# Kernel optimization log

Hardware: AMD Instinct MI355X
Metric: run time of the kernel (lower is better)

## Reference

```python
import jax, jax.numpy as jnp
import numpy as np

B, S, D = 64, 512, 768
NEG = -1e30


def setup_inputs() -> dict:
    key = jax.random.key(0)
    ks = jax.random.split(key, 20)
    def rn(k, shape, scale=0.02):
        return jax.random.normal(k, shape, dtype=jnp.float32) * scale
    ep = jax.random.randint(ks[1], (B, 3, 2), 0, S, dtype=jnp.int32)
    return {
        "encoding": jax.random.normal(ks[0], (B, S, D), dtype=jnp.float32),
        "ent_pos": jnp.sort(ep, axis=-1),
        "Ar_W": rn(ks[2], (5, D)), "Ar_b": rn(ks[3], (D,)),
        "Vr_W1": rn(ks[4], (2 * D, 512)), "Vr_b1": rn(ks[5], (512,)),
        "Vr_W2": rn(ks[6], (512, 5)), "Vr_b2": rn(ks[7], (5,)),
        "gate_W": rn(ks[8], (2 * D, D)), "gate_b": rn(ks[9], (D,)),
        "pred_W1": rn(ks[10], (3 * D, 512)), "pred_b1": rn(ks[11], (512,)),
        "pred_W2": rn(ks[12], (512, 5)), "pred_b2": rn(ks[13], (5,)),
        "proj_W": rn(ks[14], (D, 1)), "proj_b": rn(ks[15], (1,)),
    }


def reference(encoding, ent_pos, Ar_W, Ar_b, Vr_W1, Vr_b1, Vr_W2, Vr_b2,
              gate_W, gate_b, pred_W1, pred_b1, pred_W2, pred_b2, proj_W, proj_b):
    # --- entity span max-pooling (vectorized over batch & 3 entities) ---
    pos = jnp.arange(S)                                   # [S]
    start = ent_pos[..., 0:1]                             # [B,3,1]
    end = ent_pos[..., 1:2]                               # [B,3,1]
    mask = (pos >= start) & (pos <= end)                  # [B,3,S]
    ent = jnp.max(jnp.where(mask[..., None], encoding[:, None, :, :], NEG), axis=2)  # [B,3,D]
    # dropout layers are identity at inference

    def vr(a, b):  # V_r_layer: Linear(1536,512)+ReLU+Linear(512,5)+Sigmoid
        h = jax.nn.relu(jnp.concatenate([a, b], axis=-1) @ Vr_W1 + Vr_b1)
        return jax.nn.sigmoid(h @ Vr_W2 + Vr_b2)          # [B,5]

    def gate(u, e):  # gated residual update
        g = jax.nn.sigmoid(jnp.concatenate([u, e], axis=-1) @ gate_W + gate_b)
        return g * e + (1.0 - g) * u

    e1, e2, e3 = ent[:, 0], ent[:, 1], ent[:, 2]          # [B,D] each
    for _ in range(5):
        u1 = (vr(e2, e3) @ Ar_W + Ar_b) * e1
        u2 = (vr(e1, e3) @ Ar_W + Ar_b) * e2
        u3 = (vr(e1, e2) @ Ar_W + Ar_b) * e3
        e1, e2, e3 = gate(u1, e1), gate(u2, e2), gate(u3, e3)
    final_ent = jnp.stack([e1, e2, e3], axis=1)           # [B,3,D]

    # predict_layer on the ORIGINAL pooled entity embeddings (per source code)
    flat = ent.reshape(B, 3 * D)
    rel = jax.nn.relu(flat @ pred_W1 + pred_b1) @ pred_W2 + pred_b2  # [B,5]
    ent_score = jax.nn.sigmoid(ent @ proj_W + proj_b)[..., 0]       # [B,3]
    return rel, ent_score, final_ent
```

## Files before the change

kernel.cpp:

```cpp
#include <hip/hip_runtime.h>
#include <hip/hip_bf16.h>
#include <math.h>

#define NEGF (-1e30f)

#define P_OFF   0u
#define ENT_OFF 1179648u
#define EA_OFF  1327104u
#define EB_OFF  1474560u
#define SP_OFF  1622016u
#define PP_OFF  1637376u

__device__ __forceinline__ float sigmoidf_(float x){ return 1.0f/(1.0f+expf(-x)); }

__global__ __launch_bounds__(192) void k_spanmax_partial(
    const float* __restrict__ enc, const int* __restrict__ ent_pos, float* __restrict__ ws)
{
    int bi = blockIdx.y; int c = blockIdx.x; int t = threadIdx.x;
    int b = bi/3;
    int st = ent_pos[bi*2+0], en = ent_pos[bi*2+1];
    int r0 = max(st, c*64), r1 = min(en, c*64+63);
    float4 m = make_float4(NEGF,NEGF,NEGF,NEGF);
    const float4* e4 = (const float4*)enc + (size_t)b*512*192 + t;
    int r = r0;
    for (; r+3<=r1; r+=4){
        float4 v0 = e4[(size_t)(r  )*192];
        float4 v1 = e4[(size_t)(r+1)*192];
        float4 v2 = e4[(size_t)(r+2)*192];
        float4 v3 = e4[(size_t)(r+3)*192];
        m.x=fmaxf(m.x,fmaxf(fmaxf(v0.x,v1.x),fmaxf(v2.x,v3.x)));
        m.y=fmaxf(m.y,fmaxf(fmaxf(v0.y,v1.y),fmaxf(v2.y,v3.y)));
        m.z=fmaxf(m.z,fmaxf(fmaxf(v0.z,v1.z),fmaxf(v2.z,v3.z)));
        m.w=fmaxf(m.w,fmaxf(fmaxf(v0.w,v1.w),fmaxf(v2.w,v3.w)));
    }
    for (; r<=r1; ++r){
        float4 v = e4[(size_t)r*192];
        m.x=fmaxf(m.x,v.x); m.y=fmaxf(m.y,v.y); m.z=fmaxf(m.z,v.z); m.w=fmaxf(m.w,v.w);
    }
    ((float4*)(ws+P_OFF))[(bi*8+c)*192 + t] = m;
}

__global__ __launch_bounds__(256) void k_spanmax_reduce(
    const float* __restrict__ projW, const float* __restrict__ projb,
    float* __restrict__ ws, float* __restrict__ out)
{
    __shared__ float red[256];
    int bi = blockIdx.x; int t = threadIdx.x;
    float local = 0.f;
    if (t < 192){
        float4 m = make_float4(NEGF,NEGF,NEGF,NEGF);
        const float4* p4 = (const float4*)(ws+P_OFF);
        for (int c=0;c<8;++c){
            float4 v = p4[(bi*8+c)*192+t];
            m.x=fmaxf(m.x,v.x); m.y=fmaxf(m.y,v.y); m.z=fmaxf(m.z,v.z); m.w=fmaxf(m.w,v.w);
        }
        ((float4*)(ws+ENT_OFF))[bi*192+t] = m;
        ((float4*)(ws+EA_OFF))[bi*192+t] = m;
        float4 w = ((const float4*)projW)[t];
        local = m.x*w.x + m.y*w.y + m.z*w.z + m.w*w.w;
    }
    red[t]=local; __syncthreads();
    for (int off=128; off>0; off>>=1){ if (t<off) red[t]+=red[t+off]; __syncthreads(); }
    if (t==0) out[320 + bi] = sigmoidf_(red[0] + projb[0]);
}

__global__ __launch_bounds__(256) void k_pred_part(
    const float* __restrict__ predW1, float* __restrict__ ws)
{
    int ct = blockIdx.x, rb = blockIdx.y, ks = blockIdx.z;
    int tx = threadIdx.x & 31, ty = threadIdx.x >> 5;
    int row = rb*8+ty, col = ct*32+tx;
    const float* A = ws + ENT_OFF + (size_t)row*2304 + ks*288;
    const float* W = predW1 + (size_t)(ks*288)*512 + col;
    float acc = 0.f;
    #pragma unroll 4
    for (int k=0;k<288;++k){ acc = fmaf(A[k], W[(size_t)k*512], acc); }
    ws[PP_OFF + ((size_t)(ks*64+row))*512 + col] = acc;
}

__global__ __launch_bounds__(256) void k_pred_fin(
    const float* __restrict__ pb1, const float* __restrict__ predW2,
    const float* __restrict__ pb2, float* __restrict__ ws, float* __restrict__ out)
{
    __shared__ float ph[512];
    __shared__ float red[256];
    int b = blockIdx.x, t = threadIdx.x;
    for (int c = t; c < 512; c += 256){
        float s = 0.f;
        for (int ks=0;ks<8;++ks) s += ws[PP_OFF + ((size_t)(ks*64+b))*512 + c];
        ph[c] = fmaxf(s + pb1[c], 0.f);
    }
    __syncthreads();
    for (int c=0;c<5;++c){
        float local = ph[t]*predW2[t*5+c] + ph[t+256]*predW2[(t+256)*5+c];
        red[t]=local; __syncthreads();
        for (int off=128; off>0; off>>=1){ if (t<off) red[t]+=red[t+off]; __syncthreads(); }
        if (t==0) out[b*5+c] = red[0] + pb2[c];
        __syncthreads();
    }
}

__global__ __launch_bounds__(256) void k_vr_fused(
    const float* __restrict__ W1, const float* __restrict__ b1,
    const float* __restrict__ W2, const float* __restrict__ eSrc,
    float* __restrict__ ws)
{
    __shared__ float eL[4608];
    __shared__ float red[16*16*17];
    int ct = blockIdx.x, bg = blockIdx.y;
    int t = threadIdx.x;
    int b0 = bg*2;
    const float* eBase = eSrc + (size_t)b0*2304;
    for (int idx=t; idx<4608; idx+=256) eL[idx] = eBase[idx];
    __syncthreads();

    int tp = t & 15;
    int kq = t >> 4;
    int c0 = ct*64;
    int col = c0 + 4*tp;
    const float* Wp = W1 + (size_t)(kq*96)*512 + col;
    int off1 = (kq<8) ? (768 + kq*96) : (1536 + (kq-8)*96);
    int off2 = (kq<8) ? (      kq*96) : (768  + (kq-8)*96);
    const float* pP0 = eL + off1;
    const float* pQ0 = eL + off2;
    const float* pP1 = eL + 2304 + off1;
    const float* pQ1 = eL + 2304 + off2;
    float aP0[4]={0,0,0,0}, aQ0[4]={0,0,0,0}, aP1[4]={0,0,0,0}, aQ1[4]={0,0,0,0};
    #pragma unroll 8
    for (int i=0;i<96;++i){
        float4 w = *(const float4*)(Wp + (size_t)i*512);
        float p0 = pP0[i], q0 = pQ0[i], p1 = pP1[i], q1 = pQ1[i];
        aP0[0]=fmaf(p0,w.x,aP0[0]); aP0[1]=fmaf(p0,w.y,aP0[1]); aP0[2]=fmaf(p0,w.z,aP0[2]); aP0[3]=fmaf(p0,w.w,aP0[3]);
        aQ0[0]=fmaf(q0,w.x,aQ0[0]); aQ0[1]=fmaf(q0,w.y,aQ0[1]); aQ0[2]=fmaf(q0,w.z,aQ0[2]); aQ0[3]=fmaf(q0,w.w,aQ0[3]);
        aP1[0]=fmaf(p1,w.x,aP1[0]); aP1[1]=fmaf(p1,w.y,aP1[1]); aP1[2]=fmaf(p1,w.z,aP1[2]); aP1[3]=fmaf(p1,w.w,aP1[3]);
        aQ1[0]=fmaf(q1,w.x,aQ1[0]); aQ1[1]=fmaf(q1,w.y,aQ1[1]); aQ1[2]=fmaf(q1,w.z,aQ1[2]); aQ1[3]=fmaf(q1,w.w,aQ1[3]);
    }
    float* rp = red + (kq*16 + tp)*17;
    #pragma unroll
    for (int c=0;c<4;++c){ rp[c]=aP0[c]; rp[4+c]=aQ0[c]; rp[8+c]=aP1[c]; rp[12+c]=aQ1[c]; }
    __syncthreads();

    if (t < 128){
        int bb = t >> 6;
        int tc = t & 63;
        int tp2 = tc >> 2, c = tc & 3;
        int base = bb*8;
        float SP1=0,SP2=0,SQ1=0,SQ2=0;
        #pragma unroll
        for (int k=0;k<8;++k){
            SP1 += red[(k*16+tp2)*17 + base + c];
            SQ1 += red[(k*16+tp2)*17 + base + 4 + c];
            SP2 += red[((k+8)*16+tp2)*17 + base + c];
            SQ2 += red[((k+8)*16+tp2)*17 + base + 4 + c];
        }
        int cc = c0 + tc;
        float bv = b1[cc];
        float h0 = fmaxf(SP1+SP2+bv, 0.f);
        float h1 = fmaxf(SQ1+SP2+bv, 0.f);
        float h2 = fmaxf(SQ1+SQ2+bv, 0.f);
        float w20 = W2[cc*5+0], w21 = W2[cc*5+1], w22 = W2[cc*5+2], w23 = W2[cc*5+3], w24 = W2[cc*5+4];
        float pr[15] = { h0*w20,h0*w21,h0*w22,h0*w23,h0*w24,
                         h1*w20,h1*w21,h1*w22,h1*w23,h1*w24,
                         h2*w20,h2*w21,h2*w22,h2*w23,h2*w24 };
        #pragma unroll
        for (int j=0;j<15;++j){
            float v = pr[j];
            v += __shfl_down(v, 32);
            v += __shfl_down(v, 16);
            v += __shfl_down(v, 8);
            v += __shfl_down(v, 4);
            v += __shfl_down(v, 2);
            v += __shfl_down(v, 1);
            pr[j] = v;
        }
        if (tc == 0){
            float* sp = ws + SP_OFF + ((size_t)ct*192 + (size_t)(b0+bb)*3)*5;
            #pragma unroll
            for (int j=0;j<15;++j) sp[j] = pr[j];
        }
    }
}

__global__ __launch_bounds__(256) void k_gate_fused(
    const float* __restrict__ gW, const float* __restrict__ gb,
    const float* __restrict__ ArW, const float* __restrict__ Arb,
    const float* __restrict__ Vb2,
    const float* __restrict__ eSrc, float* __restrict__ eDst,
    float* __restrict__ ws, float* __restrict__ finalOut)
{
    __shared__ float eL[4608];
    __shared__ float uL[4608];
    __shared__ float red[16*16*25];
    __shared__ float sL[32];
    int ct = blockIdx.x, bg = blockIdx.y;
    int t = threadIdx.x;
    int b0 = bg*2;
    const float* eBase = eSrc + (size_t)b0*2304;
    for (int idx=t; idx<4608; idx+=256) eL[idx] = eBase[idx];
    if (t < 30){
        int bb = t/15, pc = t%15, cc = pc%5;
        int row = (b0+bb)*3 + pc/5;
        float pre = Vb2[cc];
        #pragma unroll
        for (int q=0;q<8;++q) pre += ws[SP_OFF + ((size_t)q*192 + row)*5 + cc];
        sL[t] = sigmoidf_(pre);
    }
    __syncthreads();
    for (int idx=t; idx<4608; idx+=256){
        int r = idx / 768;
        int k = idx - r*768;
        int bb = r / 3;  int p = r - bb*3;
        const float* s = sL + bb*15 + p*5;
        float a = Arb[k] + s[0]*ArW[k] + s[1]*ArW[768+k] + s[2]*ArW[1536+k]
                         + s[3]*ArW[2304+k] + s[4]*ArW[3072+k];
        uL[idx] = a * eL[idx];
    }
    __syncthreads();

    int tp = t & 15, kq = t >> 4;
    int c0 = ct*64;
    int col = c0 + 4*tp;
    const float* Wp = gW + (size_t)(kq*96)*768 + col;
    const float* A = (kq<8) ? uL : eL;
    int kb = (kq & 7)*96;
    float acc[6][4];
    #pragma unroll
    for (int r=0;r<6;++r){ acc[r][0]=0.f; acc[r][1]=0.f; acc[r][2]=0.f; acc[r][3]=0.f; }
    #pragma unroll 4
    for (int i=0;i<96;++i){
        float4 w = *(const float4*)(Wp + (size_t)i*768);
        #pragma unroll
        for (int r=0;r<6;++r){
            float a = A[r*768 + kb + i];
            acc[r][0] = fmaf(a, w.x, acc[r][0]);
            acc[r][1] = fmaf(a, w.y, acc[r][1]);
            acc[r][2] = fmaf(a, w.z, acc[r][2]);
            acc[r][3] = fmaf(a, w.w, acc[r][3]);
        }
    }
    float* rp = red + (kq*16+tp)*25;
    #pragma unroll
    for (int r=0;r<6;++r){
        rp[r*4+0]=acc[r][0]; rp[r*4+1]=acc[r][1]; rp[r*4+2]=acc[r][2]; rp[r*4+3]=acc[r][3];
    }
    __syncthreads();

    for (int o=t; o<384; o+=256){
        int tc = o & 63, rr = o >> 6;
        int tp2 = tc >> 2, c = tc & 3;
        int bb = rr/3, p = rr - bb*3;
        float gp = 0.f;
        #pragma unroll
        for (int k=0;k<16;++k) gp += red[(k*16+tp2)*25 + rr*4 + c];
        int jc = c0 + tc;
        float g = sigmoidf_(gp + gb[jc]);
        float e = eL[bb*2304 + p*768 + jc];
        float u = uL[bb*2304 + p*768 + jc];
        float val = g*e + (1.f-g)*u;
        size_t oi = ((size_t)(b0+bb)*3 + p)*768 + jc;
        eDst[oi] = val;
        if (finalOut) finalOut[oi] = val;
    }
}

extern "C" void kernel_launch(void* const* d_in, const int* in_sizes, int n_in,
                              void* d_out, int out_size, void* d_ws, size_t ws_size,
                              hipStream_t stream)
{
    const float* enc     = (const float*)d_in[0];
    const int*   ent_pos = (const int*)d_in[1];
    const float* ArW     = (const float*)d_in[2];
    const float* Arb     = (const float*)d_in[3];
    const float* VrW1    = (const float*)d_in[4];
    const float* Vrb1    = (const float*)d_in[5];
    const float* VrW2    = (const float*)d_in[6];
    const float* Vrb2    = (const float*)d_in[7];
    const float* gateW   = (const float*)d_in[8];
    const float* gateb   = (const float*)d_in[9];
    const float* predW1  = (const float*)d_in[10];
    const float* predb1  = (const float*)d_in[11];
    const float* predW2  = (const float*)d_in[12];
    const float* predb2  = (const float*)d_in[13];
    const float* projW   = (const float*)d_in[14];
    const float* projb   = (const float*)d_in[15];
    float* out = (float*)d_out;
    float* ws  = (float*)d_ws;

    hipLaunchKernelGGL(k_spanmax_partial, dim3(8,192), dim3(192), 0, stream, enc, ent_pos, ws);
    hipLaunchKernelGGL(k_spanmax_reduce, dim3(192), dim3(256), 0, stream, projW, projb, ws, out);
    hipLaunchKernelGGL(k_pred_part, dim3(16,8,8), dim3(256), 0, stream, predW1, ws);
    hipLaunchKernelGGL(k_pred_fin, dim3(64), dim3(256), 0, stream, predb1, predW2, predb2, ws, out);
    for (int it=0; it<5; ++it){
        float* eS = ws + ((it&1)==0 ? EA_OFF : EB_OFF);
        float* eD = ws + ((it&1)==0 ? EB_OFF : EA_OFF);
        hipLaunchKernelGGL(k_vr_fused,   dim3(8,32),  dim3(256), 0, stream, VrW1, Vrb1, VrW2, eS, ws);
        hipLaunchKernelGGL(k_gate_fused, dim3(12,32), dim3(256), 0, stream, gateW, gateb, ArW, Arb, Vrb2,
                           eS, eD, ws, (it==4) ? (out+512) : (float*)nullptr);
    }
}
```

Before: 165.0 us.

## Fuse all stages into one persistent cooperative kernel with grid syncs

Replaces the 14 separate kernel launches (span max, reduce, pred part/fin, and five vr/gate iterations) with a single cooperative kernel of 256 blocks of 512 threads that uses grid.sync between phases. The pred MLP is restructured so each block handles 4 batches by a 128-column strip and completes the second layer locally, and the gate phase now covers 128 columns per block with 192 blocks. The aim is to remove launch gaps between many small dependent kernels. The cost is fewer blocks (one per CU), grid-wide barriers, and idle blocks in phases that use only 64 or 192 of them.

After: 575.9 us. 249% more time.

```diff
diff --git a/kernel.cpp b/kernel.cpp
--- a/kernel.cpp
+++ b/kernel.cpp
@@ -1,265 +1,301 @@
 #include <hip/hip_runtime.h>
-#include <hip/hip_bf16.h>
+#include <hip/hip_cooperative_groups.h>
 #include <math.h>
 
+namespace cg = cooperative_groups;
+
 #define NEGF (-1e30f)
 
-#define P_OFF   0u
-#define ENT_OFF 1179648u
-#define EA_OFF  1327104u
-#define EB_OFF  1474560u
-#define SP_OFF  1622016u
-#define PP_OFF  1637376u
+#define P_OFF    0u
+#define ENT_OFF  1179648u
+#define EA_OFF   1327104u
+#define EB_OFF   1474560u
+#define SP_OFF   1622016u
+#define PRED_OFF 1629696u
 
 __device__ __forceinline__ float sigmoidf_(float x){ return 1.0f/(1.0f+expf(-x)); }
 
-__global__ __launch_bounds__(192) void k_spanmax_partial(
-    const float* __restrict__ enc, const int* __restrict__ ent_pos, float* __restrict__ ws)
+__global__ __launch_bounds__(512, 1) void k_mega(
+    const float* __restrict__ enc, const int* __restrict__ ent_pos,
+    const float* __restrict__ ArW, const float* __restrict__ Arb,
+    const float* __restrict__ VrW1, const float* __restrict__ Vrb1,
+    const float* __restrict__ VrW2, const float* __restrict__ Vrb2,
+    const float* __restrict__ gW, const float* __restrict__ gb,
+    const float* __restrict__ pW1, const float* __restrict__ pb1,
+    const float* __restrict__ pW2, const float* __restrict__ pb2,
+    const float* __restrict__ projW, const float* __restrict__ projb,
+    float* __restrict__ out, float* __restrict__ ws)
 {
-    int bi = blockIdx.y; int c = blockIdx.x; int t = threadIdx.x;
-    int b = bi/3;
-    int st = ent_pos[bi*2+0], en = ent_pos[bi*2+1];
-    int r0 = max(st, c*64), r1 = min(en, c*64+63);
-    float4 m = make_float4(NEGF,NEGF,NEGF,NEGF);
-    const float4* e4 = (const float4*)enc + (size_t)b*512*192 + t;
-    int r = r0;
-    for (; r+3<=r1; r+=4){
-        float4 v0 = e4[(size_t)(r  )*192];
-        float4 v1 = e4[(size_t)(r+1)*192];
-        float4 v2 = e4[(size_t)(r+2)*192];
-        float4 v3 = e4[(size_t)(r+3)*192];
-        m.x=fmaxf(m.x,fmaxf(fmaxf(v0.x,v1.x),fmaxf(v2.x,v3.x)));
-        m.y=fmaxf(m.y,fmaxf(fmaxf(v0.y,v1.y),fmaxf(v2.y,v3.y)));
-        m.z=fmaxf(m.z,fmaxf(fmaxf(v0.z,v1.z),fmaxf(v2.z,v3.z)));
-        m.w=fmaxf(m.w,fmaxf(fmaxf(v0.w,v1.w),fmaxf(v2.w,v3.w)));
+    cg::grid_group grid = cg::this_grid();
+    __shared__ float smem[22048];
+    const int blk = blockIdx.x;
+    const int t = threadIdx.x;
+
+    {
+        int grp = t / 192;
+        int lane = t - grp*192;
+        if (grp < 2){
+            #pragma unroll
+            for (int i=0; i<3; ++i){
+                int v = blk*6 + grp*3 + i;
+                int bi = v >> 3, c = v & 7;
+                int b = bi/3;
+                int st = ent_pos[bi*2+0], en = ent_pos[bi*2+1];
+                int r0 = max(st, c*64), r1 = min(en, c*64+63);
+                float4 m = make_float4(NEGF,NEGF,NEGF,NEGF);
+                const float4* e4 = (const float4*)enc + (size_t)b*512*192 + lane;
+                int r = r0;
+                for (; r+3<=r1; r+=4){
+                    float4 v0 = e4[(size_t)(r  )*192];
+                    float4 v1 = e4[(size_t)(r+1)*192];
+                    float4 v2 = e4[(size_t)(r+2)*192];
+                    float4 v3 = e4[(size_t)(r+3)*192];
+                    m.x=fmaxf(m.x,fmaxf(fmaxf(v0.x,v1.x),fmaxf(v2.x,v3.x)));
+                    m.y=fmaxf(m.y,fmaxf(fmaxf(v0.y,v1.y),fmaxf(v2.y,v3.y)));
+                    m.z=fmaxf(m.z,fmaxf(fmaxf(v0.z,v1.z),fmaxf(v2.z,v3.z)));
+                    m.w=fmaxf(m.w,fmaxf(fmaxf(v0.w,v1.w),fmaxf(v2.w,v3.w)));
+                }
+                for (; r<=r1; ++r){
+                    float4 v0 = e4[(size_t)r*192];
+                    m.x=fmaxf(m.x,v0.x); m.y=fmaxf(m.y,v0.y);
+                    m.z=fmaxf(m.z,v0.z); m.w=fmaxf(m.w,v0.w);
+                }
+                ((float4*)(ws+P_OFF))[(bi*8+c)*192 + lane] = m;
+            }
+        }
     }
-    for (; r<=r1; ++r){
-        float4 v = e4[(size_t)r*192];
-        m.x=fmaxf(m.x,v.x); m.y=fmaxf(m.y,v.y); m.z=fmaxf(m.z,v.z); m.w=fmaxf(m.w,v.w);
+    grid.sync();
+
+    if (blk < 192){
+        int bi = blk;
+        float* red = smem;
+        float local = 0.f;
+        if (t < 192){
+            float4 m = make_float4(NEGF,NEGF,NEGF,NEGF);
+            const float4* p4 = (const float4*)(ws+P_OFF);
+            for (int c=0;c<8;++c){
+                float4 v = p4[(bi*8+c)*192+t];
+                m.x=fmaxf(m.x,v.x); m.y=fmaxf(m.y,v.y); m.z=fmaxf(m.z,v.z); m.w=fmaxf(m.w,v.w);
+            }
+            ((float4*)(ws+ENT_OFF))[bi*192+t] = m;
+            ((float4*)(ws+EA_OFF))[bi*192+t] = m;
+            float4 w = ((const float4*)projW)[t];
+            local = m.x*w.x + m.y*w.y + m.z*w.z + m.w*w.w;
+        }
+        if (t < 256) red[t] = (t<192) ? local : 0.f;
+        __syncthreads();
+        for (int off=128; off>0; off>>=1){ if (t<off) red[t]+=red[t+off]; __syncthreads(); }
+        if (t==0) out[320 + bi] = sigmoidf_(red[0] + projb[0]);
     }
-    ((float4*)(ws+P_OFF))[(bi*8+c)*192 + t] = m;
-}
-
-__global__ __launch_bounds__(256) void k_spanmax_reduce(
-    const float* __restrict__ projW, const float* __restrict__ projb,
-    float* __restrict__ ws, float* __restrict__ out)
-{
-    __shared__ float red[256];
-    int bi = blockIdx.x; int t = threadIdx.x;
-    float local = 0.f;
-    if (t < 192){
-        float4 m = make_float4(NEGF,NEGF,NEGF,NEGF);
-        const float4* p4 = (const float4*)(ws+P_OFF);
-        for (int c=0;c<8;++c){
-            float4 v = p4[(bi*8+c)*192+t];
-            m.x=fmaxf(m.x,v.x); m.y=fmaxf(m.y,v.y); m.z=fmaxf(m.z,v.z); m.w=fmaxf(m.w,v.w);
-        }
-        ((float4*)(ws+ENT_OFF))[bi*192+t] = m;
-        ((float4*)(ws+EA_OFF))[bi*192+t] = m;
-        float4 w = ((const float4*)projW)[t];
-        local = m.x*w.x + m.y*w.y + m.z*w.z + m.w*w.w;
+    grid.sync();
+
+    if (blk < 64){
+        int bq = blk >> 2, strip = blk & 3;
+        int b0 = bq*4;
+        float* entL = smem;
+        float* red2 = smem + 9216;
+        float* hL   = smem + 11264;
+        const float* A = ws + ENT_OFF + (size_t)b0*2304;
+        for (int i=t; i<9216; i+=512) entL[i] = A[i];
+        __syncthreads();
+        {
+            int c = t & 127, q = t >> 7;
+            int col = strip*128 + c;
+            const float* W = pW1 + (size_t)(q*576)*512 + col;
+            float acc0=0,acc1=0,acc2=0,acc3=0;
+            const float* a0 = entL + q*576;
+            #pragma unroll 4
+            for (int k=0;k<576;++k){
+                float w = W[(size_t)k*512];
+                acc0 = fmaf(a0[k],        w, acc0);
+                acc1 = fmaf(a0[2304+k],   w, acc1);
+                acc2 = fmaf(a0[4608+k],   w, acc2);
+                acc3 = fmaf(a0[6912+k],   w, acc3);
+            }
+            float* rp = red2 + (size_t)q*512 + c;
+            rp[0]=acc0; rp[128]=acc1; rp[256]=acc2; rp[384]=acc3;
+        }
+        __syncthreads();
+        {
+            int bb = t >> 7, c = t & 127;
+            int col = strip*128 + c;
+            float h = red2[bb*128+c] + red2[512+bb*128+c] + red2[1024+bb*128+c] + red2[1536+bb*128+c];
+            hL[bb*128+c] = fmaxf(h + pb1[col], 0.f);
+        }
+        __syncthreads();
+        if (t < 20){
+            int bb = t/5, j = t%5;
+            float s = 0.f;
+            for (int cc=0; cc<128; ++cc)
+                s += hL[bb*128+cc] * pW2[(strip*128+cc)*5 + j];
+            ws[PRED_OFF + (size_t)((b0+bb)*4 + strip)*5 + j] = s;
+        }
     }
-    red[t]=local; __syncthreads();
-    for (int off=128; off>0; off>>=1){ if (t<off) red[t]+=red[t+off]; __syncthreads(); }
-    if (t==0) out[320 + bi] = sigmoidf_(red[0] + projb[0]);
-}
-
-__global__ __launch_bounds__(256) void k_pred_part(
-    const float* __restrict__ predW1, float* __restrict__ ws)
-{
-    int ct = blockIdx.x, rb = blockIdx.y, ks = blockIdx.z;
-    int tx = threadIdx.x & 31, ty = threadIdx.x >> 5;
-    int row = rb*8+ty, col = ct*32+tx;
-    const float* A = ws + ENT_OFF + (size_t)row*2304 + ks*288;
-    const float* W = predW1 + (size_t)(ks*288)*512 + col;
-    float acc = 0.f;
-    #pragma unroll 4
-    for (int k=0;k<288;++k){ acc = fmaf(A[k], W[(size_t)k*512], acc); }
-    ws[PP_OFF + ((size_t)(ks*64+row))*512 + col] = acc;
-}
-
-__global__ __launch_bounds__(256) void k_pred_fin(
-    const float* __restrict__ pb1, const float* __restrict__ predW2,
-    const float* __restrict__ pb2, float* __restrict__ ws, float* __restrict__ out)
-{
-    __shared__ float ph[512];
-    __shared__ float red[256];
-    int b = blockIdx.x, t = threadIdx.x;
-    for (int c = t; c < 512; c += 256){
-        float s = 0.f;
-        for (int ks=0;ks<8;++ks) s += ws[PP_OFF + ((size_t)(ks*64+b))*512 + c];
-        ph[c] = fmaxf(s + pb1[c], 0.f);
-    }
-    __syncthreads();
-    for (int c=0;c<5;++c){
-        float local = ph[t]*predW2[t*5+c] + ph[t+256]*predW2[(t+256)*5+c];
-        red[t]=local; __syncthreads();
-        for (int off=128; off>0; off>>=1){ if (t<off) red[t]+=red[t+off]; __syncthreads(); }
-        if (t==0) out[b*5+c] = red[0] + pb2[c];
-        __syncthreads();
-    }
-}
-
-__global__ __launch_bounds__(256) void k_vr_fused(
-    const float* __restrict__ W1, const float* __restrict__ b1,
-    const float* __restrict__ W2, const float* __restrict__ eSrc,
-    float* __restrict__ ws)
-{
-    __shared__ float eL[4608];
-    __shared__ float red[16*16*17];
-    int ct = blockIdx.x, bg = blockIdx.y;
-    int t = threadIdx.x;
-    int b0 = bg*2;
-    const float* eBase = eSrc + (size_t)b0*2304;
-    for (int idx=t; idx<4608; idx+=256) eL[idx] = eBase[idx];
-    __syncthreads();
-
-    int tp = t & 15;
-    int kq = t >> 4;
-    int c0 = ct*64;
-    int col = c0 + 4*tp;
-    const float* Wp = W1 + (size_t)(kq*96)*512 + col;
-    int off1 = (kq<8) ? (768 + kq*96) : (1536 + (kq-8)*96);
-    int off2 = (kq<8) ? (      kq*96) : (768  + (kq-8)*96);
-    const float* pP0 = eL + off1;
-    const float* pQ0 = eL + off2;
-    const float* pP1 = eL + 2304 + off1;
-    const float* pQ1 = eL + 2304 + off2;
-    float aP0[4]={0,0,0,0}, aQ0[4]={0,0,0,0}, aP1[4]={0,0,0,0}, aQ1[4]={0,0,0,0};
-    #pragma unroll 8
-    for (int i=0;i<96;++i){
-        float4 w = *(const float4*)(Wp + (size_t)i*512);
-        float p0 = pP0[i], q0 = pQ0[i], p1 = pP1[i], q1 = pQ1[i];
-        aP0[0]=fmaf(p0,w.x,aP0[0]); aP0[1]=fmaf(p0,w.y,aP0[1]); aP0[2]=fmaf(p0,w.z,aP0[2]); aP0[3]=fmaf(p0,w.w,aP0[3]);
-        aQ0[0]=fmaf(q0,w.x,aQ0[0]); aQ0[1]=fmaf(q0,w.y,aQ0[1]); aQ0[2]=fmaf(q0,w.z,aQ0[2]); aQ0[3]=fmaf(q0,w.w,aQ0[3]);
-        aP1[0]=fmaf(p1,w.x,aP1[0]); aP1[1]=fmaf(p1,w.y,aP1[1]); aP1[2]=fmaf(p1,w.z,aP1[2]); aP1[3]=fmaf(p1,w.w,aP1[3]);
-        aQ1[0]=fmaf(q1,w.x,aQ1[0]); aQ1[1]=fmaf(q1,w.y,aQ1[1]); aQ1[2]=fmaf(q1,w.z,aQ1[2]); aQ1[3]=fmaf(q1,w.w,aQ1[3]);
-    }
-    float* rp = red + (kq*16 + tp)*17;
-    #pragma unroll
-    for (int c=0;c<4;++c){ rp[c]=aP0[c]; rp[4+c]=aQ0[c]; rp[8+c]=aP1[c]; rp[12+c]=aQ1[c]; }
-    __syncthreads();
-
-    if (t < 128){
-        int bb = t >> 6;
-        int tc = t & 63;
-        int tp2 = tc >> 2, c = tc & 3;
-        int base = bb*8;
-        float SP1=0,SP2=0,SQ1=0,SQ2=0;
-        #pragma unroll
-        for (int k=0;k<8;++k){
-            SP1 += red[(k*16+tp2)*17 + base + c];
-            SQ1 += red[(k*16+tp2)*17 + base + 4 + c];
-            SP2 += red[((k+8)*16+tp2)*17 + base + c];
-            SQ2 += red[((k+8)*16+tp2)*17 + base + 4 + c];
-        }
-        int cc = c0 + tc;
-        float bv = b1[cc];
-        float h0 = fmaxf(SP1+SP2+bv, 0.f);
-        float h1 = fmaxf(SQ1+SP2+bv, 0.f);
-        float h2 = fmaxf(SQ1+SQ2+bv, 0.f);
-        float w20 = W2[cc*5+0], w21 = W2[cc*5+1], w22 = W2[cc*5+2], w23 = W2[cc*5+3], w24 = W2[cc*5+4];
-        float pr[15] = { h0*w20,h0*w21,h0*w22,h0*w23,h0*w24,
-                         h1*w20,h1*w21,h1*w22,h1*w23,h1*w24,
-                         h2*w20,h2*w21,h2*w22,h2*w23,h2*w24 };
-        #pragma unroll
-        for (int j=0;j<15;++j){
-            float v = pr[j];
-            v += __shfl_down(v, 32);
-            v += __shfl_down(v, 16);
-            v += __shfl_down(v, 8);
-            v += __shfl_down(v, 4);
-            v += __shfl_down(v, 2);
-            v += __shfl_down(v, 1);
-            pr[j] = v;
-        }
-        if (tc == 0){
-            float* sp = ws + SP_OFF + ((size_t)ct*192 + (size_t)(b0+bb)*3)*5;
-            #pragma unroll
-            for (int j=0;j<15;++j) sp[j] = pr[j];
-        }
-    }
-}
-
-__global__ __launch_bounds__(256) void k_gate_fused(
-    const float* __restrict__ gW, const float* __restrict__ gb,
-    const float* __restrict__ ArW, const float* __restrict__ Arb,
-    const float* __restrict__ Vb2,
-    const float* __restrict__ eSrc, float* __restrict__ eDst,
-    float* __restrict__ ws, float* __restrict__ finalOut)
-{
-    __shared__ float eL[4608];
-    __shared__ float uL[4608];
-    __shared__ float red[16*16*25];
-    __shared__ float sL[32];
-    int ct = blockIdx.x, bg = blockIdx.y;
-    int t = threadIdx.x;
-    int b0 = bg*2;
-    const float* eBase = eSrc + (size_t)b0*2304;
-    for (int idx=t; idx<4608; idx+=256) eL[idx] = eBase[idx];
-    if (t < 30){
-        int bb = t/15, pc = t%15, cc = pc%5;
-        int row = (b0+bb)*3 + pc/5;
-        float pre = Vb2[cc];
-        #pragma unroll
-        for (int q=0;q<8;++q) pre += ws[SP_OFF + ((size_t)q*192 + row)*5 + cc];
-        sL[t] = sigmoidf_(pre);
-    }
-    __syncthreads();
-    for (int idx=t; idx<4608; idx+=256){
-        int r = idx / 768;
-        int k = idx - r*768;
-        int bb = r / 3;  int p = r - bb*3;
-        const float* s = sL + bb*15 + p*5;
-        float a = Arb[k] + s[0]*ArW[k] + s[1]*ArW[768+k] + s[2]*ArW[1536+k]
-                         + s[3]*ArW[2304+k] + s[4]*ArW[3072+k];
-        uL[idx] = a * eL[idx];
-    }
-    __syncthreads();
-
-    int tp = t & 15, kq = t >> 4;
-    int c0 = ct*64;
-    int col = c0 + 4*tp;
-    const float* Wp = gW + (size_t)(kq*96)*768 + col;
-    const float* A = (kq<8) ? uL : eL;
-    int kb = (kq & 7)*96;
-    float acc[6][4];
-    #pragma unroll
-    for (int r=0;r<6;++r){ acc[r][0]=0.f; acc[r][1]=0.f; acc[r][2]=0.f; acc[r][3]=0.f; }
-    #pragma unroll 4
-    for (int i=0;i<96;++i){
-        float4 w = *(const float4*)(Wp + (size_t)i*768);
-        #pragma unroll
-        for (int r=0;r<6;++r){
-            float a = A[r*768 + kb + i];
-            acc[r][0] = fmaf(a, w.x, acc[r][0]);
-            acc[r][1] = fmaf(a, w.y, acc[r][1]);
-            acc[r][2] = fmaf(a, w.z, acc[r][2]);
-            acc[r][3] = fmaf(a, w.w, acc[r][3]);
-        }
-    }
-    float* rp = red + (kq*16+tp)*25;
-    #pragma unroll
-    for (int r=0;r<6;++r){
-        rp[r*4+0]=acc[r][0]; rp[r*4+1]=acc[r][1]; rp[r*4+2]=acc[r][2]; rp[r*4+3]=acc[r][3];
-    }
-    __syncthreads();
-
-    for (int o=t; o<384; o+=256){
-        int tc = o & 63, rr = o >> 6;
-        int tp2 = tc >> 2, c = tc & 3;
-        int bb = rr/3, p = rr - bb*3;
-        float gp = 0.f;
-        #pragma unroll
-        for (int k=0;k<16;++k) gp += red[(k*16+tp2)*25 + rr*4 + c];
-        int jc = c0 + tc;
-        float g = sigmoidf_(gp + gb[jc]);
-        float e = eL[bb*2304 + p*768 + jc];
-        float u = uL[bb*2304 + p*768 + jc];
-        float val = g*e + (1.f-g)*u;
-        size_t oi = ((size_t)(b0+bb)*3 + p)*768 + jc;
-        eDst[oi] = val;
-        if (finalOut) finalOut[oi] = val;
+    grid.sync();
+
+    for (int it=0; it<5; ++it){
+        const float* eS = ws + ((it&1)==0 ? EA_OFF : EB_OFF);
+        float*       eD = ws + ((it&1)==0 ? EB_OFF : EA_OFF);
+
+        {
+            float* eL   = smem;
+            float* redv = smem + 4608;
+            int ct = blk >> 5, bg = blk & 31;
+            int b0 = bg*2;
+            const float* eBase = eS + (size_t)b0*2304;
+            for (int idx=t; idx<4608; idx+=512) eL[idx] = eBase[idx];
+            if (it==0 && blk < 64 && t >= 256 && t < 261){
+                int j = t-256;
+                float s = pb2[j];
+                for (int q=0;q<4;++q) s += ws[PRED_OFF + (size_t)(blk*4+q)*5 + j];
+                out[blk*5+j] = s;
+            }
+            __syncthreads();
+            if (t < 256){
+                int tp = t & 15;
+                int kq = t >> 4;
+                int c0 = ct*64;
+                int col = c0 + 4*tp;
+                const float* Wp = VrW1 + (size_t)(kq*96)*512 + col;
+                int off1 = (kq<8) ? (768 + kq*96) : (1536 + (kq-8)*96);
+                int off2 = (kq<8) ? (      kq*96) : (768  + (kq-8)*96);
+                const float* pP0 = eL + off1;
+                const float* pQ0 = eL + off2;
+                const float* pP1 = eL + 2304 + off1;
+                const float* pQ1 = eL + 2304 + off2;
+                float aP0[4]={0,0,0,0}, aQ0[4]={0,0,0,0}, aP1[4]={0,0,0,0}, aQ1[4]={0,0,0,0};
+                #pragma unroll 8
+                for (int i=0;i<96;++i){
+                    float4 w = *(const float4*)(Wp + (size_t)i*512);
+                    float p0 = pP0[i], q0 = pQ0[i], p1 = pP1[i], q1 = pQ1[i];
+                    aP0[0]=fmaf(p0,w.x,aP0[0]); aP0[1]=fmaf(p0,w.y,aP0[1]); aP0[2]=fmaf(p0,w.z,aP0[2]); aP0[3]=fmaf(p0,w.w,aP0[3]);
+                    aQ0[0]=fmaf(q0,w.x,aQ0[0]); aQ0[1]=fmaf(q0,w.y,aQ0[1]); aQ0[2]=fmaf(q0,w.z,aQ0[2]); aQ0[3]=fmaf(q0,w.w,aQ0[3]);
+                    aP1[0]=fmaf(p1,w.x,aP1[0]); aP1[1]=fmaf(p1,w.y,aP1[1]); aP1[2]=fmaf(p1,w.z,aP1[2]); aP1[3]=fmaf(p1,w.w,aP1[3]);
+                    aQ1[0]=fmaf(q1,w.x,aQ1[0]); aQ1[1]=fmaf(q1,w.y,aQ1[1]); aQ1[2]=fmaf(q1,w.z,aQ1[2]); aQ1[3]=fmaf(q1,w.w,aQ1[3]);
+                }
+                float* rp = redv + (kq*16 + tp)*17;
+                #pragma unroll
+                for (int c=0;c<4;++c){ rp[c]=aP0[c]; rp[4+c]=aQ0[c]; rp[8+c]=aP1[c]; rp[12+c]=aQ1[c]; }
+            }
+            __syncthreads();
+            if (t < 128){
+                int bb = t >> 6;
+                int tc = t & 63;
+                int tp2 = tc >> 2, c = tc & 3;
+                int base = bb*8;
+                int c0 = ct*64;
+                float SP1=0,SP2=0,SQ1=0,SQ2=0;
+                #pragma unroll
+                for (int k=0;k<8;++k){
+                    SP1 += redv[(k*16+tp2)*17 + base + c];
+                    SQ1 += redv[(k*16+tp2)*17 + base + 4 + c];
+                    SP2 += redv[((k+8)*16+tp2)*17 + base + c];
+                    SQ2 += redv[((k+8)*16+tp2)*17 + base + 4 + c];
+                }
+                int cc = c0 + tc;
+                float bv = Vrb1[cc];
+                float h0 = fmaxf(SP1+SP2+bv, 0.f);
+                float h1 = fmaxf(SQ1+SP2+bv, 0.f);
+                float h2 = fmaxf(SQ1+SQ2+bv, 0.f);
+                float w20 = VrW2[cc*5+0], w21 = VrW2[cc*5+1], w22 = VrW2[cc*5+2], w23 = VrW2[cc*5+3], w24 = VrW2[cc*5+4];
+                float pr[15] = { h0*w20,h0*w21,h0*w22,h0*w23,h0*w24,
+                                 h1*w20,h1*w21,h1*w22,h1*w23,h1*w24,
+                                 h2*w20,h2*w21,h2*w22,h2*w23,h2*w24 };
+                #pragma unroll
+                for (int j=0;j<15;++j){
+                    float v = pr[j];
+                    v += __shfl_down(v, 32);
+                    v += __shfl_down(v, 16);
+                    v += __shfl_down(v, 8);
+                    v += __shfl_down(v, 4);
+                    v += __shfl_down(v, 2);
+                    v += __shfl_down(v, 1);
+                    pr[j] = v;
+                }
+                if (tc == 0){
+                    float* sp = ws + SP_OFF + ((size_t)ct*192 + (size_t)(b0+bb)*3)*5;
+                    #pragma unroll
+                    for (int j=0;j<15;++j) sp[j] = pr[j];
+                }
+            }
+        }
+        grid.sync();
+
+        if (blk < 192){
+            float* eL   = smem;
+            float* uL   = smem + 4608;
+            float* redg = smem + 9216;
+            float* sL   = smem + 22016;
+            int ct = blk / 32, bg = blk % 32;
+            int b0 = bg*2;
+            const float* eBase = eS + (size_t)b0*2304;
+            for (int idx=t; idx<4608; idx+=512) eL[idx] = eBase[idx];
+            if (t < 30){
+                int bb = t/15, pc = t%15, cc = pc%5;
+                int row = (b0+bb)*3 + pc/5;
+                float pre = Vrb2[cc];
+                #pragma unroll
+                for (int q=0;q<8;++q) pre += ws[SP_OFF + ((size_t)q*192 + row)*5 + cc];
+                sL[t] = sigmoidf_(pre);
+            }
+            __syncthreads();
+            for (int idx=t; idx<4608; idx+=512){
+                int r = idx / 768;
+                int k = idx - r*768;
+                int bb = r / 3;  int p = r - bb*3;
+                const float* s = sL + bb*15 + p*5;
+                float a = Arb[k] + s[0]*ArW[k] + s[1]*ArW[768+k] + s[2]*ArW[1536+k]
+                                 + s[3]*ArW[2304+k] + s[4]*ArW[3072+k];
+                uL[idx] = a * eL[idx];
+            }
+            __syncthreads();
+            {
+                int tp = t & 31, kq = t >> 5;
+                int c0 = ct*128;
+                int col = c0 + 4*tp;
+                const float* Wp = gW + (size_t)(kq*96)*768 + col;
+                const float* A = (kq<8) ? uL : eL;
+                int kb = (kq & 7)*96;
+                float acc[6][4];
+                #pragma unroll
+                for (int r=0;r<6;++r){ acc[r][0]=0.f; acc[r][1]=0.f; acc[r][2]=0.f; acc[r][3]=0.f; }
+                #pragma unroll 4
+                for (int i=0;i<96;++i){
+                    float4 w = *(const float4*)(Wp + (size_t)i*768);
+                    #pragma unroll
+                    for (int r=0;r<6;++r){
+                        float a = A[r*768 + kb + i];
+                        acc[r][0] = fmaf(a, w.x, acc[r][0]);
+                        acc[r][1] = fmaf(a, w.y, acc[r][1]);
+                        acc[r][2] = fmaf(a, w.z, acc[r][2]);
+                        acc[r][3] = fmaf(a, w.w, acc[r][3]);
+                    }
+                }
+                float* rp = redg + (kq*32+tp)*25;
+                #pragma unroll
+                for (int r=0;r<6;++r){
+                    rp[r*4+0]=acc[r][0]; rp[r*4+1]=acc[r][1]; rp[r*4+2]=acc[r][2]; rp[r*4+3]=acc[r][3];
+                }
+            }
+            __syncthreads();
+            for (int o=t; o<768; o+=512){
+                int tc = o & 127, rr = o >> 7;
+                int tp2 = tc >> 2, c = tc & 3;
+                int bb = rr/3, p = rr - bb*3;
+                float gp = 0.f;
+                #pragma unroll
+                for (int k=0;k<16;++k) gp += redg[(k*32+tp2)*25 + rr*4 + c];
+                int jc = ct*128 + tc;
+                float g = sigmoidf_(gp + gb[jc]);
+                float e = eL[bb*2304 + p*768 + jc];
+                float u = uL[bb*2304 + p*768 + jc];
+                float val = g*e + (1.f-g)*u;
+                size_t oi = ((size_t)(b0+bb)*3 + p)*768 + jc;
+                eD[oi] = val;
+                if (it==4) out[512 + oi] = val;
+            }
+        }
+        grid.sync();
     }
 }
 
@@ -286,15 +322,14 @@
     float* out = (float*)d_out;
     float* ws  = (float*)d_ws;
 
-    hipLaunchKernelGGL(k_spanmax_partial, dim3(8,192), dim3(192), 0, stream, enc, ent_pos, ws);
-    hipLaunchKernelGGL(k_spanmax_reduce, dim3(192), dim3(256), 0, stream, projW, projb, ws, out);
-    hipLaunchKernelGGL(k_pred_part, dim3(16,8,8), dim3(256), 0, stream, predW1, ws);
-    hipLaunchKernelGGL(k_pred_fin, dim3(64), dim3(256), 0, stream, predb1, predW2, predb2, ws, out);
-    for (int it=0; it<5; ++it){
-        float* eS = ws + ((it&1)==0 ? EA_OFF : EB_OFF);
-        float* eD = ws + ((it&1)==0 ? EB_OFF : EA_OFF);
-        hipLaunchKernelGGL(k_vr_fused,   dim3(8,32),  dim3(256), 0, stream, VrW1, Vrb1, VrW2, eS, ws);
-        hipLaunchKernelGGL(k_gate_fused, dim3(12,32), dim3(256), 0, stream, gateW, gateb, ArW, Arb, Vrb2,
-                           eS, eD, ws, (it==4) ? (out+512) : (float*)nullptr);
-    }
+    void* args[] = {
+        (void*)&enc, (void*)&ent_pos,
+        (void*)&ArW, (void*)&Arb,
+        (void*)&VrW1, (void*)&Vrb1, (void*)&VrW2, (void*)&Vrb2,
+        (void*)&gateW, (void*)&gateb,
+        (void*)&predW1, (void*)&predb1, (void*)&predW2, (void*)&predb2,
+        (void*)&projW, (void*)&projb,
+        (void*)&out, (void*)&ws
+    };
+    hipLaunchCooperativeKernel((const void*)k_mega, dim3(256), dim3(512), args, 0, stream);
 }
```

## Merge span-max kernels, fold pred head into first Vr launch, widen gate tiles

Applied to the files above, without the earlier changes.

The span max-pool now runs in one block per entity with a wave-shuffle reduction for the projection score, which removes the partial/reduce kernel pair and its workspace round trip. The pred_fin head is folded into the first k_vr_fused launch as 8 extra blocks, so one launch is dropped. k_gate_fused moves to 384 threads covering 96 columns per block on a flat grid of 256 blocks instead of 12x32, which lowers how often the activations are reloaded into shared memory. The trade-off is less parallelism in span pooling for long spans and larger shared-memory use per gate block.

Result: slower. 183.8 us (+11.4%).

```diff
diff --git a/kernel.cpp b/kernel.cpp
--- a/kernel.cpp
+++ b/kernel.cpp
@@ -4,26 +4,27 @@
 
 #define NEGF (-1e30f)
 
-#define P_OFF   0u
-#define ENT_OFF 1179648u
-#define EA_OFF  1327104u
-#define EB_OFF  1474560u
-#define SP_OFF  1622016u
-#define PP_OFF  1637376u
+#define ENT_OFF  1179648u
+#define EA_OFF   1327104u
+#define EB_OFF   1474560u
+#define SP_OFF   1622016u
+#define PP_OFF   1637376u
 
 __device__ __forceinline__ float sigmoidf_(float x){ return 1.0f/(1.0f+expf(-x)); }
 
-__global__ __launch_bounds__(192) void k_spanmax_partial(
-    const float* __restrict__ enc, const int* __restrict__ ent_pos, float* __restrict__ ws)
-{
-    int bi = blockIdx.y; int c = blockIdx.x; int t = threadIdx.x;
+__global__ __launch_bounds__(192) void k_span(
+    const float* __restrict__ enc, const int* __restrict__ ent_pos,
+    const float* __restrict__ projW, const float* __restrict__ projb,
+    float* __restrict__ ws, float* __restrict__ out)
+{
+    __shared__ float red[4];
+    int bi = blockIdx.x; int t = threadIdx.x;
     int b = bi/3;
     int st = ent_pos[bi*2+0], en = ent_pos[bi*2+1];
-    int r0 = max(st, c*64), r1 = min(en, c*64+63);
     float4 m = make_float4(NEGF,NEGF,NEGF,NEGF);
     const float4* e4 = (const float4*)enc + (size_t)b*512*192 + t;
-    int r = r0;
-    for (; r+3<=r1; r+=4){
+    int r = st;
+    for (; r+3<=en; r+=4){
         float4 v0 = e4[(size_t)(r  )*192];
         float4 v1 = e4[(size_t)(r+1)*192];
         float4 v2 = e4[(size_t)(r+2)*192];
@@ -33,35 +34,23 @@
         m.z=fmaxf(m.z,fmaxf(fmaxf(v0.z,v1.z),fmaxf(v2.z,v3.z)));
         m.w=fmaxf(m.w,fmaxf(fmaxf(v0.w,v1.w),fmaxf(v2.w,v3.w)));
     }
-    for (; r<=r1; ++r){
+    for (; r<=en; ++r){
         float4 v = e4[(size_t)r*192];
         m.x=fmaxf(m.x,v.x); m.y=fmaxf(m.y,v.y); m.z=fmaxf(m.z,v.z); m.w=fmaxf(m.w,v.w);
     }
-    ((float4*)(ws+P_OFF))[(bi*8+c)*192 + t] = m;
-}
-
-__global__ __launch_bounds__(256) void k_spanmax_reduce(
-    const float* __restrict__ projW, const float* __restrict__ projb,
-    float* __restrict__ ws, float* __restrict__ out)
-{
-    __shared__ float red[256];
-    int bi = blockIdx.x; int t = threadIdx.x;
-    float local = 0.f;
-    if (t < 192){
-        float4 m = make_float4(NEGF,NEGF,NEGF,NEGF);
-        const float4* p4 = (const float4*)(ws+P_OFF);
-        for (int c=0;c<8;++c){
-            float4 v = p4[(bi*8+c)*192+t];
-            m.x=fmaxf(m.x,v.x); m.y=fmaxf(m.y,v.y); m.z=fmaxf(m.z,v.z); m.w=fmaxf(m.w,v.w);
-        }
-        ((float4*)(ws+ENT_OFF))[bi*192+t] = m;
-        ((float4*)(ws+EA_OFF))[bi*192+t] = m;
-        float4 w = ((const float4*)projW)[t];
-        local = m.x*w.x + m.y*w.y + m.z*w.z + m.w*w.w;
-    }
-    red[t]=local; __syncthreads();
-    for (int off=128; off>0; off>>=1){ if (t<off) red[t]+=red[t+off]; __syncthreads(); }
-    if (t==0) out[320 + bi] = sigmoidf_(red[0] + projb[0]);
+    ((float4*)(ws+ENT_OFF))[bi*192+t] = m;
+    ((float4*)(ws+EA_OFF))[bi*192+t] = m;
+    float4 w = ((const float4*)projW)[t];
+    float v = m.x*w.x + m.y*w.y + m.z*w.z + m.w*w.w;
+    v += __shfl_down(v, 32);
+    v += __shfl_down(v, 16);
+    v += __shfl_down(v, 8);
+    v += __shfl_down(v, 4);
+    v += __shfl_down(v, 2);
+    v += __shfl_down(v, 1);
+    if ((t & 63) == 0) red[t>>6] = v;
+    __syncthreads();
+    if (t==0) out[320 + bi] = sigmoidf_(red[0]+red[1]+red[2] + projb[0]);
 }
 
 __global__ __launch_bounds__(256) void k_pred_part(
@@ -78,37 +67,51 @@
     ws[PP_OFF + ((size_t)(ks*64+row))*512 + col] = acc;
 }
 
-__global__ __launch_bounds__(256) void k_pred_fin(
-    const float* __restrict__ pb1, const float* __restrict__ predW2,
-    const float* __restrict__ pb2, float* __restrict__ ws, float* __restrict__ out)
-{
-    __shared__ float ph[512];
-    __shared__ float red[256];
-    int b = blockIdx.x, t = threadIdx.x;
-    for (int c = t; c < 512; c += 256){
-        float s = 0.f;
-        for (int ks=0;ks<8;++ks) s += ws[PP_OFF + ((size_t)(ks*64+b))*512 + c];
-        ph[c] = fmaxf(s + pb1[c], 0.f);
-    }
-    __syncthreads();
-    for (int c=0;c<5;++c){
-        float local = ph[t]*predW2[t*5+c] + ph[t+256]*predW2[(t+256)*5+c];
-        red[t]=local; __syncthreads();
-        for (int off=128; off>0; off>>=1){ if (t<off) red[t]+=red[t+off]; __syncthreads(); }
-        if (t==0) out[b*5+c] = red[0] + pb2[c];
-        __syncthreads();
-    }
-}
-
 __global__ __launch_bounds__(256) void k_vr_fused(
     const float* __restrict__ W1, const float* __restrict__ b1,
     const float* __restrict__ W2, const float* __restrict__ eSrc,
-    float* __restrict__ ws)
+    const float* __restrict__ pb1, const float* __restrict__ pW2,
+    const float* __restrict__ pb2,
+    float* __restrict__ ws, float* __restrict__ out)
 {
     __shared__ float eL[4608];
     __shared__ float red[16*16*17];
-    int ct = blockIdx.x, bg = blockIdx.y;
+    int g = blockIdx.x;
     int t = threadIdx.x;
+    if (g >= 256){
+        int bx = g - 256;
+        int gid = t >> 5, l = t & 31;
+        int b = bx*8 + gid;
+        float acc0=0,acc1=0,acc2=0,acc3=0,acc4=0;
+        for (int c = l; c < 512; c += 32){
+            float h = 0.f;
+            #pragma unroll
+            for (int ks=0;ks<8;++ks) h += ws[PP_OFF + ((size_t)(ks*64+b))*512 + c];
+            h = fmaxf(h + pb1[c], 0.f);
+            acc0 = fmaf(h, pW2[c*5+0], acc0);
+            acc1 = fmaf(h, pW2[c*5+1], acc1);
+            acc2 = fmaf(h, pW2[c*5+2], acc2);
+            acc3 = fmaf(h, pW2[c*5+3], acc3);
+            acc4 = fmaf(h, pW2[c*5+4], acc4);
+        }
+        #pragma unroll
+        for (int s=16; s>0; s>>=1){
+            acc0 += __shfl_down(acc0, s, 32);
+            acc1 += __shfl_down(acc1, s, 32);
+            acc2 += __shfl_down(acc2, s, 32);
+            acc3 += __shfl_down(acc3, s, 32);
+            acc4 += __shfl_down(acc4, s, 32);
+        }
+        if (l == 0){
+            out[b*5+0] = acc0 + pb2[0];
+            out[b*5+1] = acc1 + pb2[1];
+            out[b*5+2] = acc2 + pb2[2];
+            out[b*5+3] = acc3 + pb2[3];
+            out[b*5+4] = acc4 + pb2[4];
+        }
+        return;
+    }
+    int ct = g & 7, bg = g >> 3;
     int b0 = bg*2;
     const float* eBase = eSrc + (size_t)b0*2304;
     for (int idx=t; idx<4608; idx+=256) eL[idx] = eBase[idx];
@@ -181,7 +184,7 @@
     }
 }
 
-__global__ __launch_bounds__(256) void k_gate_fused(
+__global__ __launch_bounds__(384) void k_gate_fused(
     const float* __restrict__ gW, const float* __restrict__ gb,
     const float* __restrict__ ArW, const float* __restrict__ Arb,
     const float* __restrict__ Vb2,
@@ -190,13 +193,14 @@
 {
     __shared__ float eL[4608];
     __shared__ float uL[4608];
-    __shared__ float red[16*16*25];
+    __shared__ float red[16*24*25];
     __shared__ float sL[32];
-    int ct = blockIdx.x, bg = blockIdx.y;
+    int g = blockIdx.x;
     int t = threadIdx.x;
+    int ct = g & 7, bg = g >> 3;
     int b0 = bg*2;
     const float* eBase = eSrc + (size_t)b0*2304;
-    for (int idx=t; idx<4608; idx+=256) eL[idx] = eBase[idx];
+    for (int idx=t; idx<4608; idx+=384) eL[idx] = eBase[idx];
     if (t < 30){
         int bb = t/15, pc = t%15, cc = pc%5;
         int row = (b0+bb)*3 + pc/5;
@@ -206,7 +210,7 @@
         sL[t] = sigmoidf_(pre);
     }
     __syncthreads();
-    for (int idx=t; idx<4608; idx+=256){
+    for (int idx=t; idx<4608; idx+=384){
         int r = idx / 768;
         int k = idx - r*768;
         int bb = r / 3;  int p = r - bb*3;
@@ -217,8 +221,8 @@
     }
     __syncthreads();
 
-    int tp = t & 15, kq = t >> 4;
-    int c0 = ct*64;
+    int kq = t / 24, tp = t - kq*24;
+    int c0 = ct*96;
     int col = c0 + 4*tp;
     const float* Wp = gW + (size_t)(kq*96)*768 + col;
     const float* A = (kq<8) ? uL : eL;
@@ -238,25 +242,25 @@
             acc[r][3] = fmaf(a, w.w, acc[r][3]);
         }
     }
-    float* rp = red + (kq*16+tp)*25;
+    float* rp = red + (kq*24+tp)*25;
     #pragma unroll
     for (int r=0;r<6;++r){
         rp[r*4+0]=acc[r][0]; rp[r*4+1]=acc[r][1]; rp[r*4+2]=acc[r][2]; rp[r*4+3]=acc[r][3];
     }
     __syncthreads();
 
-    for (int o=t; o<384; o+=256){
-        int tc = o & 63, rr = o >> 6;
+    for (int o=t; o<576; o+=384){
+        int rr = o / 96, tc = o - rr*96;
         int tp2 = tc >> 2, c = tc & 3;
         int bb = rr/3, p = rr - bb*3;
         float gp = 0.f;
         #pragma unroll
-        for (int k=0;k<16;++k) gp += red[(k*16+tp2)*25 + rr*4 + c];
+        for (int k=0;k<16;++k) gp += red[(k*24+tp2)*25 + rr*4 + c];
         int jc = c0 + tc;
-        float g = sigmoidf_(gp + gb[jc]);
+        float gv = sigmoidf_(gp + gb[jc]);
         float e = eL[bb*2304 + p*768 + jc];
         float u = uL[bb*2304 + p*768 + jc];
-        float val = g*e + (1.f-g)*u;
+        float val = gv*e + (1.f-gv)*u;
         size_t oi = ((size_t)(b0+bb)*3 + p)*768 + jc;
         eDst[oi] = val;
         if (finalOut) finalOut[oi] = val;
@@ -286,15 +290,14 @@
     float* out = (float*)d_out;
     float* ws  = (float*)d_ws;
 
-    hipLaunchKernelGGL(k_spanmax_partial, dim3(8,192), dim3(192), 0, stream, enc, ent_pos, ws);
-    hipLaunchKernelGGL(k_spanmax_reduce, dim3(192), dim3(256), 0, stream, projW, projb, ws, out);
+    hipLaunchKernelGGL(k_span, dim3(192), dim3(192), 0, stream, enc, ent_pos, projW, projb, ws, out);
     hipLaunchKernelGGL(k_pred_part, dim3(16,8,8), dim3(256), 0, stream, predW1, ws);
-    hipLaunchKernelGGL(k_pred_fin, dim3(64), dim3(256), 0, stream, predb1, predW2, predb2, ws, out);
     for (int it=0; it<5; ++it){
         float* eS = ws + ((it&1)==0 ? EA_OFF : EB_OFF);
         float* eD = ws + ((it&1)==0 ? EB_OFF : EA_OFF);
-        hipLaunchKernelGGL(k_vr_fused,   dim3(8,32),  dim3(256), 0, stream, VrW1, Vrb1, VrW2, eS, ws);
-        hipLaunchKernelGGL(k_gate_fused, dim3(12,32), dim3(256), 0, stream, gateW, gateb, ArW, Arb, Vrb2,
+        hipLaunchKernelGGL(k_vr_fused, dim3(it==0 ? 264 : 256), dim3(256), 0, stream,
+                           VrW1, Vrb1, VrW2, eS, predb1, predW2, predb2, ws, out);
+        hipLaunchKernelGGL(k_gate_fused, dim3(256), dim3(384), 0, stream, gateW, gateb, ArW, Arb, Vrb2,
                            eS, eD, ws, (it==4) ? (out+512) : (float*)nullptr);
     }
 }
```
